# Kernel optimization log

Measured on AMD Instinct MI355X. Metric: run time of the kernel, lower is better.

The kernel has to match this reference:

```python
import jax, jax.numpy as jnp
import numpy as np

N = 50000
E = 800000
IN = 128
HID = 128
OUT = 128
HEADS = 8
EPS = 1e-5
NEG_SLOPE = 0.2


def _gat_conv(x, src, dst, W, a_src, a_dst, b, concat):
    """PyG-style GATConv (eval mode, self-loops already appended to src/dst).
    W: [Fin, H*C], a_src/a_dst: [H, C], b: [H*C] or [C]."""
    n = x.shape[0]
    H, C = a_src.shape
    h = (x @ W).reshape(n, H, C)                      # [N,H,C]
    al_s = jnp.einsum('nhc,hc->nh', h, a_src)         # [N,H]
    al_d = jnp.einsum('nhc,hc->nh', h, a_dst)         # [N,H]
    e = jax.nn.leaky_relu(al_s[src] + al_d[dst], NEG_SLOPE)  # [E',H]
    m = jax.ops.segment_max(e, dst, num_segments=n)   # per-dst softmax (stable)
    ex = jnp.exp(e - m[dst])
    s = jax.ops.segment_sum(ex, dst, num_segments=n)
    alpha = ex / s[dst]                               # [E',H]
    out = jax.ops.segment_sum(h[src] * alpha[..., None], dst, num_segments=n)
    out = out.reshape(n, H * C) if concat else out[:, 0, :]
    return out + b


def _layernorm(x, g, b):
    mu = x.mean(-1, keepdims=True)
    var = ((x - mu) ** 2).mean(-1, keepdims=True)
    return (x - mu) * jax.lax.rsqrt(var + EPS) * g + b


def setup_inputs() -> dict:
    key = jax.random.key(0)
    ks = jax.random.split(key, 24)
    d = {}
    d['x'] = jax.random.normal(ks[0], (N, IN), jnp.float32)
    d['edge_index'] = jax.random.randint(ks[1], (2, E), 0, N)
    C = HID // HEADS
    # layer 0: in -> hidden, 8 heads, concat
    d['W0'] = jax.random.normal(ks[2], (IN, HID)) * 0.05
    d['a_src0'] = jax.random.normal(ks[3], (HEADS, C)) * 0.05
    d['a_dst0'] = jax.random.normal(ks[4], (HEADS, C)) * 0.05
    d['b0'] = jnp.zeros((HID,), jnp.float32)
    d['g0'] = jnp.ones((HID,), jnp.float32)
    d['be0'] = jnp.zeros((HID,), jnp.float32)
    # layer 1: hidden -> hidden, 8 heads, concat
    d['W1'] = jax.random.normal(ks[5], (HID, HID)) * 0.05
    d['a_src1'] = jax.random.normal(ks[6], (HEADS, C)) * 0.05
    d['a_dst1'] = jax.random.normal(ks[7], (HEADS, C)) * 0.05
    d['b1'] = jnp.zeros((HID,), jnp.float32)
    d['g1'] = jnp.ones((HID,), jnp.float32)
    d['be1'] = jnp.zeros((HID,), jnp.float32)
    # layer 2: hidden -> out, 1 head, no concat
    d['W2'] = jax.random.normal(ks[8], (HID, OUT)) * 0.05
    d['a_src2'] = jax.random.normal(ks[9], (1, OUT)) * 0.05
    d['a_dst2'] = jax.random.normal(ks[10], (1, OUT)) * 0.05
    d['b2'] = jnp.zeros((OUT,), jnp.float32)
    d['g2'] = jnp.ones((OUT,), jnp.float32)
    d['be2'] = jnp.zeros((OUT,), jnp.float32)
    return d


def reference(x, edge_index, W0, a_src0, a_dst0, b0, g0, be0,
              W1, a_src1, a_dst1, b1, g1, be1,
              W2, a_src2, a_dst2, b2, g2, be2):
    n = x.shape[0]
    loops = jnp.arange(n)
    src = jnp.concatenate([edge_index[0], loops])  # add self-loops (PyG default)
    dst = jnp.concatenate([edge_index[1], loops])

    h = _gat_conv(x, src, dst, W0, a_src0, a_dst0, b0, concat=True)
    h = jax.nn.elu(_layernorm(h, g0, be0))          # dropout: eval mode -> identity
    h = _gat_conv(h, src, dst, W1, a_src1, a_dst1, b1, concat=True)
    h = jax.nn.elu(_layernorm(h, g1, be1))
    h = _gat_conv(h, src, dst, W2, a_src2, a_dst2, b2, concat=False)
    h = _layernorm(h, g2, be2)
    return h
```

## Files before the change

### kernel.cpp

```cpp
#include <hip/hip_runtime.h>
#include <hip/hip_bf16.h>

#define NN 50000
#define EE 800000
#define EP 850000
#define DD 128
#define NB 196

#define NBUCK 196
#define BCAP 8192
#define E_PER_BLK 4096
#define GEMM_BLKS 782
#define BP1_BLKS ((EP + E_PER_BLK - 1)/E_PER_BLK)

typedef __attribute__((ext_vector_type(8))) short short8;
typedef __attribute__((ext_vector_type(4))) float f32x4;

__device__ __forceinline__ float bfu(unsigned short u){ return __uint_as_float(((unsigned)u)<<16); }
__device__ __forceinline__ unsigned short f2bs(float x){
  __hip_bfloat16 h = __float2bfloat16(x);
  union { __hip_bfloat16 h; unsigned short u; } cv; cv.h = h; return cv.u;
}

__global__ void __launch_bounds__(256) prep_kernel(
    const float* __restrict__ W0, const float* __restrict__ as0, const float* __restrict__ ad0,
    const float* __restrict__ W1, const float* __restrict__ as1, const float* __restrict__ ad1,
    const float* __restrict__ W2, const float* __restrict__ as2, const float* __restrict__ ad2,
    unsigned short* __restrict__ Wmf, int* __restrict__ bcur)
{
  const int tid = threadIdx.x;
  if (blockIdx.x == 0 && tid < NBUCK) bcur[tid] = 0;
  if (blockIdx.x < 24){
    const int L = blockIdx.x >> 3, seg = blockIdx.x & 7;
    const float* W = (L == 0) ? W0 : (L == 1) ? W1 : W2;
    int idx = seg*256 + tid;
    int t = idx >> 6, lane = idx & 63;
    int c = t >> 2, kb = t & 3;
    int m = lane & 15, quad = lane >> 4;
    unsigned short out[8];
    #pragma unroll
    for (int j = 0; j < 8; j++){
      int k = kb*32 + quad*8 + j;
      out[j] = f2bs(W[(size_t)k*DD + c*16 + m]);
    }
    *(uint4*)&Wmf[(((size_t)L*36 + t)*64 + lane)*8] = *(const uint4*)out;
  } else if (blockIdx.x < 120){
    const int q = blockIdx.x - 24;
    const int wIdx = q*4 + (tid >> 6);
    const int L = wIdx >> 7, k = wIdx & 127;
    const float *W, *as, *ad; int H;
    if (L == 0){ W = W0; as = as0; ad = ad0; H = 8; }
    else if (L == 1){ W = W1; as = as1; ad = ad1; H = 8; }
    else { W = W2; as = as2; ad = ad2; H = 1; }
    const int lane = tid & 63;
    const int c0 = lane*2;
    float w0 = W[(size_t)k*DD + c0];
    float w1 = W[(size_t)k*DD + c0 + 1];
    float ps = w0*as[c0] + w1*as[c0+1];
    float pd = w0*ad[c0] + w1*ad[c0+1];
    if (H == 8){
      #pragma unroll
      for (int off = 1; off <= 4; off <<= 1){
        ps += __shfl_xor(ps, off, 64);
        pd += __shfl_xor(pd, off, 64);
      }
    } else {
      #pragma unroll
      for (int off = 1; off <= 32; off <<= 1){
        ps += __shfl_xor(ps, off, 64);
        pd += __shfl_xor(pd, off, 64);
      }
    }
    int srcLane = (lane < 8) ? lane*8 : (lane < 16 ? (lane-8)*8 : 0);
    float vs = __shfl(ps, srcLane, 64);
    float vd = __shfl(pd, srcLane, 64);
    float myv;
    if (H == 8) myv = (lane < 8) ? vs : (lane < 16 ? vd : 0.f);
    else        myv = (lane == 0) ? ps : (lane == 1 ? pd : 0.f);
    const int kb = k >> 5, quad = (k >> 3) & 3, j = k & 7;
    if (lane < 16)
      Wmf[(((size_t)L*36 + 32 + kb)*64 + quad*16 + lane)*8 + j] = f2bs(myv);
  }
}

__device__ __forceinline__ void bp1_body(int bid, const int* __restrict__ ei,
    unsigned int* __restrict__ bins, int* __restrict__ bcur, char* smem)
{
  unsigned int* st = (unsigned int*)smem;
  int* h     = (int*)(smem + 16384);
  int* lofs  = (int*)(smem + 17168);
  int* gbase = (int*)(smem + 17952);
  int* buf   = (int*)(smem + 18736);
  const int tid = threadIdx.x;
  for (int i = tid; i < NBUCK; i += 256) h[i] = 0;
  __syncthreads();

  const int e0 = bid * E_PER_BLK;
  unsigned int pk[16];
  #pragma unroll
  for (int k = 0; k < 16; k++){
    int e = e0 + k*256 + tid;
    if (e < EP){
      int s, d;
      if (e < EE){ s = ei[e]; d = ei[EE + e]; } else { s = d = e - EE; }
      int b = d >> 8;
      pk[k] = ((unsigned)s << 16) | ((unsigned)b << 8) | (unsigned)(d & 255);
      atomicAdd(&h[b], 1);
    } else pk[k] = 0xFFFFFFFFu;
  }
  __syncthreads();

  int v = (tid < NBUCK) ? h[tid] : 0;
  buf[tid] = v;
  __syncthreads();
  for (int off = 1; off < 256; off <<= 1){
    int t = (tid >= off) ? buf[tid - off] : 0;
    __syncthreads();
    buf[tid] += t;
    __syncthreads();
  }
  if (tid < NBUCK){
    lofs[tid]  = buf[tid] - v;
    gbase[tid] = (v > 0) ? atomicAdd(&bcur[tid], v) : 0;
    h[tid] = lofs[tid];
  }
  __syncthreads();

  #pragma unroll
  for (int k = 0; k < 16; k++){
    if (pk[k] != 0xFFFFFFFFu){
      int b = (pk[k] >> 8) & 255;
      int p = atomicAdd(&h[b], 1);
      st[p] = pk[k];
    }
  }
  __syncthreads();

  const int total = buf[255];
  for (int i = tid; i < total; i += 256){
    unsigned int p = st[i];
    int b = (p >> 8) & 255;
    int idx = gbase[b] + (i - lofs[b]);
    if (idx < BCAP) bins[(size_t)b * BCAP + idx] = p;
  }
}

__global__ void __launch_bounds__(256) binpass2_kernel(const unsigned int* __restrict__ bins,
    const int* __restrict__ bcur, int* __restrict__ rowStart, unsigned short* __restrict__ srcL)
{
  __shared__ int buf[256];
  __shared__ int lcnt[256];
  __shared__ int lcur[256];
  __shared__ int ebase_s, cnt_s;
  const int b = blockIdx.x;
  const int tid = threadIdx.x;

  int v = (tid < NBUCK) ? bcur[tid] : 0;
  buf[tid] = v;
  lcnt[tid] = 0;
  __syncthreads();
  for (int off = 1; off < 256; off <<= 1){
    int t = (tid >= off) ? buf[tid - off] : 0;
    __syncthreads();
    buf[tid] += t;
    __syncthreads();
  }
  if (tid == b){ ebase_s = buf[tid] - v; cnt_s = v; }
  __syncthreads();
  const int ebase = ebase_s, cnt = cnt_s;
  const unsigned int* mybins = bins + (size_t)b * BCAP;

  for (int i = tid; i < cnt; i += 256)
    atomicAdd(&lcnt[mybins[i] & 255], 1);
  __syncthreads();

  int c = lcnt[tid];
  buf[tid] = c;
  __syncthreads();
  for (int off = 1; off < 256; off <<= 1){
    int t = (tid >= off) ? buf[tid - off] : 0;
    __syncthreads();
    buf[tid] += t;
    __syncthreads();
  }
  int excl = buf[tid] - c;
  int d = (b << 8) + tid;
  if (d <= NN) rowStart[d] = ebase + excl;
  lcur[tid] = ebase + excl;
  __syncthreads();

  for (int i = tid; i < cnt; i += 256){
    unsigned int p = mybins[i];
    int pos = atomicAdd(&lcur[p & 255], 1);
    srcL[pos] = (unsigned short)(p >> 16);
  }
}

template<bool XBF16, int H>
__device__ __forceinline__ void gemm_body(int bid, const void* __restrict__ Xv,
    const unsigned short* __restrict__ Wmf,
    unsigned short* __restrict__ Hout,
    float* __restrict__ alS, float* __restrict__ alD,
    unsigned short* wl)
{
  const int tid = threadIdx.x;
  {
    const uint4* src = (const uint4*)Wmf;
    uint4* dst = (uint4*)wl;
    #pragma unroll
    for (int i = 0; i < 9; i++)
      dst[tid + i*256] = src[tid + i*256];
  }
  const int lane = tid & 63, wv = tid >> 6;
  const int r0 = bid*64 + wv*16;
  const int m = lane & 15, quad = lane >> 4;
  const int row = r0 + m;
  const bool rowOK = row < NN;

  short8 a[4];
  if (XBF16){
    const short* Xb = (const short*)Xv;
    #pragma unroll
    for (int kb = 0; kb < 4; kb++){
      if (rowOK) a[kb] = *(const short8*)&Xb[(size_t)row*DD + kb*32 + quad*8];
      else       a[kb] = (short8){0,0,0,0,0,0,0,0};
    }
  } else {
    const float* Xf = (const float*)Xv;
    #pragma unroll
    for (int kb = 0; kb < 4; kb++){
      if (rowOK){
        float4 f0 = *(const float4*)&Xf[(size_t)row*DD + kb*32 + quad*8];
        float4 f1 = *(const float4*)&Xf[(size_t)row*DD + kb*32 + quad*8 + 4];
        union { short8 v; unsigned short u[8]; } cv;
        cv.u[0]=f2bs(f0.x); cv.u[1]=f2bs(f0.y); cv.u[2]=f2bs(f0.z); cv.u[3]=f2bs(f0.w);
        cv.u[4]=f2bs(f1.x); cv.u[5]=f2bs(f1.y); cv.u[6]=f2bs(f1.z); cv.u[7]=f2bs(f1.w);
        a[kb] = cv.v;
      } else a[kb] = (short8){0,0,0,0,0,0,0,0};
    }
  }
  __syncthreads();

  f32x4 acc[9];
  #pragma unroll
  for (int c = 0; c < 9; c++) acc[c] = (f32x4){0.f,0.f,0.f,0.f};
  #pragma unroll
  for (int c = 0; c < 9; c++){
    #pragma unroll
    for (int kb = 0; kb < 4; kb++){
      short8 b = *(const short8*)&wl[((c*4 + kb)*64 + lane)*8];
      acc[c] = __builtin_amdgcn_mfma_f32_16x16x32_bf16(a[kb], b, acc[c], 0, 0, 0);
    }
  }

  #pragma unroll
  for (int r = 0; r < 4; r++){
    int rw = r0 + quad*4 + r;
    if (rw < NN){
      float v = acc[8][r];
      if (H == 8){
        if (m < 8) alS[rw*8 + m]       = v;
        else       alD[rw*8 + (m - 8)] = v;
      } else {
        if (m == 0)      alS[rw] = v;
        else if (m == 1) alD[rw] = v;
      }
    }
  }

  __syncthreads();
  unsigned short* ht = wl;
  const int lr = wv*16 + quad*4;
  #pragma unroll
  for (int c = 0; c < 8; c++){
    #pragma unroll
    for (int r = 0; r < 4; r++)
      ht[(lr + r)*136 + c*16 + m] = f2bs(acc[c][r]);
  }
  __syncthreads();
  const int r0b = bid*64;
  #pragma unroll
  for (int p = 0; p < 4; p++){
    int i = p*256 + tid;
    int lrow = i >> 4, chunk = i & 15;
    int grow = r0b + lrow;
    if (grow < NN){
      uint4 v = *(const uint4*)((const char*)ht + lrow*272 + chunk*16);
      *(uint4*)&Hout[(size_t)grow*DD + chunk*8] = v;
    }
  }
}

template<bool XBF16, int H>
__global__ void __launch_bounds__(256) gemm_mfma_kernel(const void* __restrict__ Xv,
    const unsigned short* __restrict__ Wmf,
    unsigned short* __restrict__ Hout,
    float* __restrict__ alS, float* __restrict__ alD)
{
  __shared__ unsigned short wl[36*64*8];
  gemm_body<XBF16, H>(blockIdx.x, Xv, Wmf, Hout, alS, alD, wl);
}

template<bool XBF16, int H>
__global__ void __launch_bounds__(256) gemm_bp1_kernel(const void* __restrict__ Xv,
    const unsigned short* __restrict__ Wmf,
    unsigned short* __restrict__ Hout,
    float* __restrict__ alS, float* __restrict__ alD,
    const int* __restrict__ ei, unsigned int* __restrict__ bins, int* __restrict__ bcur)
{
  __shared__ __align__(16) char smem[36*64*8*2];
  if (blockIdx.x < GEMM_BLKS)
    gemm_body<XBF16, H>(blockIdx.x, Xv, Wmf, Hout, alS, alD, (unsigned short*)smem);
  else
    bp1_body(blockIdx.x - GEMM_BLKS, ei, bins, bcur, smem);
}

template<int H, bool FINAL>
__global__ void __launch_bounds__(256) aggln_kernel(
    const int* __restrict__ rowStart, const unsigned short* __restrict__ srcL,
    const float* __restrict__ alS, const float* __restrict__ alD,
    const unsigned short* __restrict__ hB,
    const float* __restrict__ b, const float* __restrict__ g, const float* __restrict__ be,
    void* __restrict__ outv)
{
  const int lane = threadIdx.x & 63;
  const int d    = blockIdx.x*4 + (threadIdx.x >> 6);
  const int C    = DD / H;
  const int c0   = lane*2;
  const int hd   = c0 / C;
  const int start = __builtin_amdgcn_readfirstlane(rowStart[d]);
  const int end   = __builtin_amdgcn_readfirstlane(rowStart[d+1]);
  const float aldv = alD[d*H + hd];

  float ssum = 0.f, a0 = 0.f, a1 = 0.f;
  const unsigned int* __restrict__ sw = (const unsigned int*)srcL;

  #define PROC(sv) { \
    int s_ = (sv); \
    const unsigned short* hr_ = hB + (size_t)s_*DD; \
    const float* ar_ = alS + s_*H; \
    unsigned int hw_ = *(const unsigned int*)&hr_[c0]; \
    float e_ = ar_[hd] + aldv; \
    e_ = fmaxf(e_, 0.2f*e_); \
    float w_ = __expf(e_); \
    ssum += w_; \
    a0 = fmaf(__uint_as_float(hw_ << 16),          w_, a0); \
    a1 = fmaf(__uint_as_float(hw_ & 0xFFFF0000u),  w_, a1); \
  }

  int jw = start >> 1;
  if (start & 1){
    unsigned int w = sw[jw]; PROC((int)(w >> 16)); jw++;
  }
  const int jwF = end >> 1;
  for (; jw + 2 <= jwF; jw += 2){
    unsigned int w0 = sw[jw], w1 = sw[jw+1];
    PROC((int)(w0 & 0xFFFFu)); PROC((int)(w0 >> 16));
    PROC((int)(w1 & 0xFFFFu)); PROC((int)(w1 >> 16));
  }
  for (; jw < jwF; ++jw){
    unsigned int w = sw[jw];
    PROC((int)(w & 0xFFFFu)); PROC((int)(w >> 16));
  }
  if (end & 1){
    unsigned int w = sw[jwF]; PROC((int)(w & 0xFFFFu));
  }
  #undef PROC

  const float sinv = 1.f / ssum;

  float v0 = a0*sinv + b[c0], v1 = a1*sinv + b[c0+1];
  float s2 = v0 + v1;
  #pragma unroll
  for (int off = 32; off >= 1; off >>= 1) s2 += __shfl_xor(s2, off, 64);
  float mu = s2 * (1.0f/128.0f);
  float d0 = v0 - mu, d1 = v1 - mu;
  float q = d0*d0 + d1*d1;
  #pragma unroll
  for (int off = 32; off >= 1; off >>= 1) q += __shfl_xor(q, off, 64);
  float r = rsqrtf(q*(1.0f/128.0f) + 1e-5f);
  float y0 = d0*r*g[c0]   + be[c0];
  float y1 = d1*r*g[c0+1] + be[c0+1];
  if (FINAL){
    *(float2*)&((float*)outv)[(size_t)d*DD + c0] = make_float2(y0, y1);
  } else {
    y0 = y0 > 0.f ? y0 : __expf(y0) - 1.f;
    y1 = y1 > 0.f ? y1 : __expf(y1) - 1.f;
    ushort2 o; o.x = f2bs(y0); o.y = f2bs(y1);
    *(ushort2*)&((unsigned short*)outv)[(size_t)d*DD + c0] = o;
  }
}

extern "C" void kernel_launch(void* const* d_in, const int* in_sizes, int n_in,
                              void* d_out, int out_size, void* d_ws, size_t ws_size,
                              hipStream_t stream)
{
  char* w = (char*)d_ws;
  unsigned short* accB = (unsigned short*)w;     w += (size_t)NN*DD*2;
  unsigned short* hB   = (unsigned short*)w;     w += (size_t)NN*DD*2;
  float* alS      = (float*)w;                   w += (size_t)NN*8*4;
  float* alD      = (float*)w;                   w += (size_t)NN*8*4;
  unsigned short* Wmf = (unsigned short*)w;      w += (size_t)3*36*64*8*2;
  int*   rowStart = (int*)w;                     w += (size_t)(NN+1)*4;
  int*   bcur     = (int*)w;                     w += 1024;
  unsigned short* srcL = (unsigned short*)w;     w += (size_t)EP*2;
  if (ws_size < (size_t)(w - (char*)d_ws)) return;

  unsigned int* bins = (unsigned int*)accB;

  const float* x  = (const float*)d_in[0];
  const int*   ei = (const int*)d_in[1];
  const float *W0=(const float*)d_in[2], *as0=(const float*)d_in[3], *ad0=(const float*)d_in[4];
  const float *b0=(const float*)d_in[5], *g0=(const float*)d_in[6], *be0=(const float*)d_in[7];
  const float *W1=(const float*)d_in[8], *as1=(const float*)d_in[9], *ad1=(const float*)d_in[10];
  const float *b1=(const float*)d_in[11],*g1=(const float*)d_in[12],*be1=(const float*)d_in[13];
  const float *W2=(const float*)d_in[14],*as2=(const float*)d_in[15],*ad2=(const float*)d_in[16];
  const float *b2=(const float*)d_in[17],*g2=(const float*)d_in[18],*be2=(const float*)d_in[19];

  prep_kernel<<<NB, 256, 0, stream>>>(W0, as0, ad0, W1, as1, ad1, W2, as2, ad2, Wmf, bcur);

  gemm_bp1_kernel<false, 8><<<GEMM_BLKS + BP1_BLKS, 256, 0, stream>>>(
      x, Wmf, hB, alS, alD, ei, bins, bcur);
  binpass2_kernel<<<NBUCK, 256, 0, stream>>>(bins, bcur, rowStart, srcL);

  aggln_kernel<8, false><<<12500, 256, 0, stream>>>(rowStart, srcL, alS, alD, hB,
                                                    b0, g0, be0, accB);
  gemm_mfma_kernel<true, 8><<<GEMM_BLKS, 256, 0, stream>>>(accB, Wmf + (size_t)36*64*8,
                                                           hB, alS, alD);
  aggln_kernel<8, false><<<12500, 256, 0, stream>>>(rowStart, srcL, alS, alD, hB,
                                                    b1, g1, be1, accB);
  gemm_mfma_kernel<true, 1><<<GEMM_BLKS, 256, 0, stream>>>(accB, Wmf + (size_t)2*36*64*8,
                                                           hB, alS, alD);
  aggln_kernel<1, true><<<12500, 256, 0, stream>>>(rowStart, srcL, alS, alD, hB,
                                                   b2, g2, be2, d_out);
}
```

Before: 275.6 us.

## Widen binpass2 to 512 threads, reorder fused blocks, specialize GEMM tail

```diff
diff --git a/kernel.cpp b/kernel.cpp
--- a/kernel.cpp
+++ b/kernel.cpp
@@ -145,7 +145,7 @@
   }
 }
 
-__global__ void __launch_bounds__(256) binpass2_kernel(const unsigned int* __restrict__ bins,
+__global__ void __launch_bounds__(512) binpass2_kernel(const unsigned int* __restrict__ bins,
     const int* __restrict__ bcur, int* __restrict__ rowStart, unsigned short* __restrict__ srcL)
 {
   __shared__ int buf[256];
@@ -155,14 +155,17 @@
   const int b = blockIdx.x;
   const int tid = threadIdx.x;
 
-  int v = (tid < NBUCK) ? bcur[tid] : 0;
-  buf[tid] = v;
-  lcnt[tid] = 0;
+  int v = 0;
+  if (tid < 256){
+    v = (tid < NBUCK) ? bcur[tid] : 0;
+    buf[tid] = v;
+    lcnt[tid] = 0;
+  }
   __syncthreads();
   for (int off = 1; off < 256; off <<= 1){
-    int t = (tid >= off) ? buf[tid - off] : 0;
-    __syncthreads();
-    buf[tid] += t;
+    int t = (tid >= off && tid < 256) ? buf[tid - off] : 0;
+    __syncthreads();
+    if (tid < 256) buf[tid] += t;
     __syncthreads();
   }
   if (tid == b){ ebase_s = buf[tid] - v; cnt_s = v; }
@@ -170,26 +173,28 @@
   const int ebase = ebase_s, cnt = cnt_s;
   const unsigned int* mybins = bins + (size_t)b * BCAP;
 
-  for (int i = tid; i < cnt; i += 256)
+  for (int i = tid; i < cnt; i += 512)
     atomicAdd(&lcnt[mybins[i] & 255], 1);
   __syncthreads();
 
-  int c = lcnt[tid];
-  buf[tid] = c;
+  int c = 0;
+  if (tid < 256){ c = lcnt[tid]; buf[tid] = c; }
   __syncthreads();
   for (int off = 1; off < 256; off <<= 1){
-    int t = (tid >= off) ? buf[tid - off] : 0;
-    __syncthreads();
-    buf[tid] += t;
-    __syncthreads();
-  }
-  int excl = buf[tid] - c;
-  int d = (b << 8) + tid;
-  if (d <= NN) rowStart[d] = ebase + excl;
-  lcur[tid] = ebase + excl;
-  __syncthreads();
-
-  for (int i = tid; i < cnt; i += 256){
+    int t = (tid >= off && tid < 256) ? buf[tid - off] : 0;
+    __syncthreads();
+    if (tid < 256) buf[tid] += t;
+    __syncthreads();
+  }
+  if (tid < 256){
+    int excl = buf[tid] - c;
+    int d = (b << 8) + tid;
+    if (d <= NN) rowStart[d] = ebase + excl;
+    lcur[tid] = ebase + excl;
+  }
+  __syncthreads();
+
+  for (int i = tid; i < cnt; i += 512){
     unsigned int p = mybins[i];
     int pos = atomicAdd(&lcur[p & 255], 1);
     srcL[pos] = (unsigned short)(p >> 16);
@@ -215,21 +220,27 @@
   const int r0 = bid*64 + wv*16;
   const int m = lane & 15, quad = lane >> 4;
   const int row = r0 + m;
-  const bool rowOK = row < NN;
+  const bool tail = (bid == GEMM_BLKS - 1);
 
   short8 a[4];
   if (XBF16){
     const short* Xb = (const short*)Xv;
-    #pragma unroll
-    for (int kb = 0; kb < 4; kb++){
-      if (rowOK) a[kb] = *(const short8*)&Xb[(size_t)row*DD + kb*32 + quad*8];
-      else       a[kb] = (short8){0,0,0,0,0,0,0,0};
+    if (!tail){
+      #pragma unroll
+      for (int kb = 0; kb < 4; kb++)
+        a[kb] = *(const short8*)&Xb[(size_t)row*DD + kb*32 + quad*8];
+    } else {
+      #pragma unroll
+      for (int kb = 0; kb < 4; kb++){
+        if (row < NN) a[kb] = *(const short8*)&Xb[(size_t)row*DD + kb*32 + quad*8];
+        else          a[kb] = (short8){0,0,0,0,0,0,0,0};
+      }
     }
   } else {
     const float* Xf = (const float*)Xv;
     #pragma unroll
     for (int kb = 0; kb < 4; kb++){
-      if (rowOK){
+      if (!tail || row < NN){
         float4 f0 = *(const float4*)&Xf[(size_t)row*DD + kb*32 + quad*8];
         float4 f1 = *(const float4*)&Xf[(size_t)row*DD + kb*32 + quad*8 + 4];
         union { short8 v; unsigned short u[8]; } cv;
@@ -253,10 +264,10 @@
     }
   }
 
-  #pragma unroll
-  for (int r = 0; r < 4; r++){
-    int rw = r0 + quad*4 + r;
-    if (rw < NN){
+  if (!tail){
+    #pragma unroll
+    for (int r = 0; r < 4; r++){
+      int rw = r0 + quad*4 + r;
       float v = acc[8][r];
       if (H == 8){
         if (m < 8) alS[rw*8 + m]       = v;
@@ -266,6 +277,21 @@
         else if (m == 1) alD[rw] = v;
       }
     }
+  } else {
+    #pragma unroll
+    for (int r = 0; r < 4; r++){
+      int rw = r0 + quad*4 + r;
+      if (rw < NN){
+        float v = acc[8][r];
+        if (H == 8){
+          if (m < 8) alS[rw*8 + m]       = v;
+          else       alD[rw*8 + (m - 8)] = v;
+        } else {
+          if (m == 0)      alS[rw] = v;
+          else if (m == 1) alD[rw] = v;
+        }
+      }
+    }
   }
 
   __syncthreads();
@@ -279,14 +305,24 @@
   }
   __syncthreads();
   const int r0b = bid*64;
-  #pragma unroll
-  for (int p = 0; p < 4; p++){
-    int i = p*256 + tid;
-    int lrow = i >> 4, chunk = i & 15;
-    int grow = r0b + lrow;
-    if (grow < NN){
+  if (!tail){
+    #pragma unroll
+    for (int p = 0; p < 4; p++){
+      int i = p*256 + tid;
+      int lrow = i >> 4, chunk = i & 15;
       uint4 v = *(const uint4*)((const char*)ht + lrow*272 + chunk*16);
-      *(uint4*)&Hout[(size_t)grow*DD + chunk*8] = v;
+      *(uint4*)&Hout[(size_t)(r0b + lrow)*DD + chunk*8] = v;
+    }
+  } else {
+    #pragma unroll
+    for (int p = 0; p < 4; p++){
+      int i = p*256 + tid;
+      int lrow = i >> 4, chunk = i & 15;
+      int grow = r0b + lrow;
+      if (grow < NN){
+        uint4 v = *(const uint4*)((const char*)ht + lrow*272 + chunk*16);
+        *(uint4*)&Hout[(size_t)grow*DD + chunk*8] = v;
+      }
     }
   }
 }
@@ -309,10 +345,11 @@
     const int* __restrict__ ei, unsigned int* __restrict__ bins, int* __restrict__ bcur)
 {
   __shared__ __align__(16) char smem[36*64*8*2];
-  if (blockIdx.x < GEMM_BLKS)
-    gemm_body<XBF16, H>(blockIdx.x, Xv, Wmf, Hout, alS, alD, (unsigned short*)smem);
+  if (blockIdx.x < BP1_BLKS)
+    bp1_body(blockIdx.x, ei, bins, bcur, smem);
   else
-    bp1_body(blockIdx.x - GEMM_BLKS, ei, bins, bcur, smem);
+    gemm_body<XBF16, H>(blockIdx.x - BP1_BLKS, Xv, Wmf, Hout, alS, alD,
+                        (unsigned short*)smem);
 }
 
 template<int H, bool FINAL>
@@ -421,7 +458,7 @@
 
   gemm_bp1_kernel<false, 8><<<GEMM_BLKS + BP1_BLKS, 256, 0, stream>>>(
       x, Wmf, hB, alS, alD, ei, bins, bcur);
-  binpass2_kernel<<<NBUCK, 256, 0, stream>>>(bins, bcur, rowStart, srcL);
+  binpass2_kernel<<<NBUCK, 512, 0, stream>>>(bins, bcur, rowStart, srcL);
 
   aggln_kernel<8, false><<<12500, 256, 0, stream>>>(rowStart, srcL, alS, alD, hB,
                                                     b0, g0, be0, accB);
```

New measurement: 271.9 us (median of 2 runs). Within noise of the previous version (-1.3%).
